# Optimization experiments

Measured on AMD Instinct MI355X. Metric: run time of the kernel, lower is better.

## Reference

```python
import jax, jax.numpy as jnp
import numpy as np

N = 50000
E = 800000
F_IN = 128
HID = 128
OUT = 64
EPS = 1e-5


def gcn_conv(x, src, dst, deg_inv_sqrt, W, b):
    # h = x @ W  (dense transform first, like PyG GCNConv)
    h = x @ W  # [N, F_out]
    norm = deg_inv_sqrt[src] * deg_inv_sqrt[dst]  # [E+N] (self-loops included)
    msgs = norm[:, None] * h[src]  # gather + scale, [E+N, F_out]
    out = jax.ops.segment_sum(msgs, dst, num_segments=N)  # scatter-add to targets
    return out + b


def setup_inputs() -> dict:
    key = jax.random.key(0)
    ks = jax.random.split(key, 9)
    x = jax.random.normal(ks[0], (N, F_IN), dtype=jnp.float32)
    edge_index = jax.random.randint(ks[1], (2, E), 0, N, dtype=jnp.int64)
    s = 1.0 / np.sqrt(F_IN)
    W1 = jax.random.uniform(ks[2], (F_IN, HID), jnp.float32, -s, s)
    b1 = jnp.zeros((HID,), jnp.float32)
    sh = 1.0 / np.sqrt(HID)
    Wmu = jax.random.uniform(ks[3], (HID, OUT), jnp.float32, -sh, sh)
    bmu = jnp.zeros((OUT,), jnp.float32)
    Wlv = jax.random.uniform(ks[4], (HID, OUT), jnp.float32, -sh, sh)
    blv = jnp.zeros((OUT,), jnp.float32)
    gamma = jnp.ones((HID,), jnp.float32)
    beta = jnp.zeros((HID,), jnp.float32)
    return {"x": x, "edge_index": edge_index, "W1": W1, "b1": b1,
            "gamma": gamma, "beta": beta, "Wmu": Wmu, "bmu": bmu,
            "Wlv": Wlv, "blv": blv}


def reference(x, edge_index, W1, b1, gamma, beta, Wmu, bmu, Wlv, blv):
    # Add self-loops (GCNConv default) and compute symmetric normalization once.
    loop = jnp.arange(N, dtype=edge_index.dtype)
    src = jnp.concatenate([edge_index[0], loop])
    dst = jnp.concatenate([edge_index[1], loop])
    deg = jax.ops.segment_sum(jnp.ones_like(dst, dtype=x.dtype), dst, num_segments=N)
    deg_inv_sqrt = jnp.where(deg > 0, jax.lax.rsqrt(deg), 0.0)

    h = jax.nn.relu(gcn_conv(x, src, dst, deg_inv_sqrt, W1, b1))
    # per-node LayerNorm over feature dim
    mean = jnp.mean(h, axis=-1, keepdims=True)
    var = jnp.var(h, axis=-1, keepdims=True)
    h = (h - mean) * jax.lax.rsqrt(var + EPS) * gamma + beta

    mu = gcn_conv(h, src, dst, deg_inv_sqrt, Wmu, bmu)
    logvar = gcn_conv(h, src, dst, deg_inv_sqrt, Wlv, blv)
    return mu, logvar
```

## Files before the change

### kernel.cpp

```cpp
#include <hip/hip_runtime.h>

#define NN 50000
#define EE 800000
#define FF 128
#define OO 64
#define EPSF 1e-5f
#define SCB 196
#define EBLK 3125
#define GBLK 391

typedef unsigned int uint;
typedef unsigned short ushort;
typedef __attribute__((ext_vector_type(8))) short short8;
typedef __attribute__((ext_vector_type(4))) float f32x4;

__device__ __forceinline__ float bflo(uint v) { return __uint_as_float(v << 16); }
__device__ __forceinline__ float bfhi(uint v) { return __uint_as_float(v & 0xFFFF0000u); }
__device__ __forceinline__ uint f2bf(float f) {
  uint b = __float_as_uint(f);
  return (b + 0x7FFFu + ((b >> 16) & 1u)) >> 16;
}
__device__ __forceinline__ uint pack2(float x, float y) { return f2bf(x) | (f2bf(y) << 16); }

__device__ __forceinline__ int eidx(const void* ei, long long pos, int f64) {
  if (f64) return (int)((const long long*)ei)[pos];
  return ((const int*)ei)[pos];
}

__global__ void k_init(const void* ei, int* flag, int* cnt) {
  int i = blockIdx.x * 256 + threadIdx.x;
  if (i < NN) cnt[i] = 0;
  if (i == 0) {
    const int* p = (const int*)ei;
    int any = 0;
    for (int j = 1; j < 128; j += 2) any |= p[j];
    *flag = (any == 0) ? 1 : 0;
  }
}

__global__ void k_deg_rank(const void* ei, const int* __restrict__ flag,
                           int* __restrict__ cnt, int* __restrict__ rank) {
  int e = blockIdx.x * 256 + threadIdx.x;
  if (e >= EE) return;
  int f64 = *flag;
  int d = eidx(ei, (long long)EE + e, f64);
  rank[e] = atomicAdd(&cnt[d], 1);
}

__global__ __launch_bounds__(256) void k_dis_part(const int* __restrict__ cnt,
                                                  float* __restrict__ dis,
                                                  int* __restrict__ bsum) {
  int i = blockIdx.x * 256 + threadIdx.x;
  int v = (i < NN) ? cnt[i] : 0;
  if (i < NN) dis[i] = rsqrtf((float)(v + 1));
  int s = v;
#pragma unroll
  for (int m = 1; m < 64; m <<= 1) s += __shfl_xor(s, m);
  __shared__ int ws[4];
  if ((threadIdx.x & 63) == 0) ws[threadIdx.x >> 6] = s;
  __syncthreads();
  if (threadIdx.x == 0) bsum[blockIdx.x] = ws[0] + ws[1] + ws[2] + ws[3];
}

__global__ __launch_bounds__(256) void k_scan_tops(const int* __restrict__ bsum,
                                                   int* __restrict__ boff,
                                                   int* __restrict__ rowptr) {
  __shared__ int s[256];
  int tid = threadIdx.x;
  int v = (tid < SCB) ? bsum[tid] : 0;
  s[tid] = v;
  __syncthreads();
  for (int off = 1; off < 256; off <<= 1) {
    int t = (tid >= off) ? s[tid - off] : 0;
    __syncthreads();
    s[tid] += t;
    __syncthreads();
  }
  if (tid < SCB) boff[tid] = s[tid] - v;
  if (tid == 255) rowptr[NN] = s[255];
}

__global__ __launch_bounds__(256) void k_scan_write(const int* __restrict__ cnt,
                                                    const int* __restrict__ boff,
                                                    int* __restrict__ rowptr) {
  int blk = blockIdx.x, tid = threadIdx.x;
  int i = blk * 256 + tid;
  int v = (i < NN) ? cnt[i] : 0;
  int lane = tid & 63, wid = tid >> 6;
  int inc = v;
#pragma unroll
  for (int off = 1; off < 64; off <<= 1) {
    int t = __shfl_up(inc, off);
    if (lane >= off) inc += t;
  }
  __shared__ int wsum[4];
  if (lane == 63) wsum[wid] = inc;
  __syncthreads();
  int wadd = 0;
  for (int wj = 0; wj < wid; ++wj) wadd += wsum[wj];
  int exc = inc - v + wadd + boff[blk];
  if (i < NN) rowptr[i] = exc;
}

__device__ __forceinline__ int wt_idx(int c, int k) {
  return c * 128 + (k ^ ((c & 7) << 3));
}

__global__ __launch_bounds__(256) void k_scatter_gemm1(
    const void* ei, const int* __restrict__ flag, const float* __restrict__ dis,
    const int* __restrict__ rowptr, const int* __restrict__ rank,
    int2* __restrict__ cw,
    const float* __restrict__ X, const float* __restrict__ W,
    ushort* __restrict__ T) {
  __shared__ ushort Wt[FF * FF];
  if (blockIdx.x >= GBLK) {
    int e = (blockIdx.x - GBLK) * 256 + threadIdx.x;
    if (e >= EE) return;
    int f64 = *flag;
    int s = eidx(ei, e, f64);
    int d = eidx(ei, (long long)EE + e, f64);
    int p = rowptr[d] + rank[e];
    int2 v;
    v.x = s;
    v.y = __float_as_int(dis[s] * dis[d]);
    cw[p] = v;
    return;
  }
  for (int i = threadIdx.x; i < FF * FF; i += 256) {
    int k = i >> 7, c = i & 127;
    Wt[wt_idx(c, k)] = (ushort)f2bf(W[i]);
  }
  __syncthreads();
  int l = threadIdx.x & 63, wv = threadIdx.x >> 6;
  int rbase = blockIdx.x * 128 + wv * 32;
  int lr = l & 15, lk = (l >> 4) << 3;
  f32x4 acc[2][8] = {};
#pragma unroll
  for (int kb = 0; kb < 4; ++kb) {
    int kk = kb * 32 + lk;
    short8 a[2];
#pragma unroll
    for (int rt = 0; rt < 2; ++rt) {
      int row = min(rbase + rt * 16 + lr, NN - 1);
      const float4* ap = (const float4*)(X + (size_t)row * FF + kk);
      float4 x0 = ap[0], x1 = ap[1];
      a[rt][0] = (short)f2bf(x0.x); a[rt][1] = (short)f2bf(x0.y);
      a[rt][2] = (short)f2bf(x0.z); a[rt][3] = (short)f2bf(x0.w);
      a[rt][4] = (short)f2bf(x1.x); a[rt][5] = (short)f2bf(x1.y);
      a[rt][6] = (short)f2bf(x1.z); a[rt][7] = (short)f2bf(x1.w);
    }
#pragma unroll
    for (int ct = 0; ct < 8; ++ct) {
      int c = ct * 16 + lr;
      short8 b = *(const short8*)&Wt[wt_idx(c, kk)];
      acc[0][ct] = __builtin_amdgcn_mfma_f32_16x16x32_bf16(a[0], b, acc[0][ct], 0, 0, 0);
      acc[1][ct] = __builtin_amdgcn_mfma_f32_16x16x32_bf16(a[1], b, acc[1][ct], 0, 0, 0);
    }
  }
  int rl = (l >> 4) * 4;
#pragma unroll
  for (int rt = 0; rt < 2; ++rt)
#pragma unroll
    for (int reg = 0; reg < 4; ++reg) {
      int row = rbase + rt * 16 + rl + reg;
      if (row < NN) {
#pragma unroll
        for (int ct = 0; ct < 8; ++ct)
          T[(size_t)row * FF + ct * 16 + lr] = (ushort)f2bf(acc[rt][ct][reg]);
      }
    }
}

__global__ __launch_bounds__(256) void k_gemm2(const ushort* __restrict__ A,
                                               const float* __restrict__ Wmu,
                                               const float* __restrict__ bmu,
                                               const float* __restrict__ Wlv,
                                               const float* __restrict__ blv,
                                               float* __restrict__ out) {
  __shared__ ushort Wt[FF * FF];
  __shared__ float sb[FF];
  for (int i = threadIdx.x; i < FF * FF; i += 256) {
    int k = i >> 7, c = i & 127;
    float v = (c < OO) ? Wmu[k * OO + c] : Wlv[k * OO + (c - OO)];
    Wt[wt_idx(c, k)] = (ushort)f2bf(v);
  }
  if (threadIdx.x < FF)
    sb[threadIdx.x] = (threadIdx.x < OO) ? bmu[threadIdx.x] : blv[threadIdx.x - OO];
  __syncthreads();
  int l = threadIdx.x & 63, wv = threadIdx.x >> 6;
  int rbase = blockIdx.x * 128 + wv * 32;
  int lr = l & 15, lk = (l >> 4) << 3;
  f32x4 acc[2][8] = {};
#pragma unroll
  for (int kb = 0; kb < 4; ++kb) {
    int kk = kb * 32 + lk;
    short8 a[2];
#pragma unroll
    for (int rt = 0; rt < 2; ++rt) {
      int row = min(rbase + rt * 16 + lr, NN - 1);
      a[rt] = *(const short8*)(A + (size_t)row * FF + kk);
    }
#pragma unroll
    for (int ct = 0; ct < 8; ++ct) {
      int c = ct * 16 + lr;
      short8 b = *(const short8*)&Wt[wt_idx(c, kk)];
      acc[0][ct] = __builtin_amdgcn_mfma_f32_16x16x32_bf16(a[0], b, acc[0][ct], 0, 0, 0);
      acc[1][ct] = __builtin_amdgcn_mfma_f32_16x16x32_bf16(a[1], b, acc[1][ct], 0, 0, 0);
    }
  }
  int rl = (l >> 4) * 4;
#pragma unroll
  for (int rt = 0; rt < 2; ++rt)
#pragma unroll
    for (int reg = 0; reg < 4; ++reg) {
      int row = rbase + rt * 16 + rl + reg;
      if (row < NN) {
#pragma unroll
        for (int ct = 0; ct < 8; ++ct) {
          int c = ct * 16 + lr;
          float v = acc[rt][ct][reg] + sb[c];
          if (ct < 4) out[(size_t)row * OO + c] = v;
          else out[(size_t)NN * OO + (size_t)row * OO + (c - OO)] = v;
        }
      }
    }
}

template <int LN>
__global__ __launch_bounds__(256) void k_gather(const int* __restrict__ rowptr,
                                                const int2* __restrict__ cw,
                                                const float* __restrict__ dis,
                                                const ushort* __restrict__ feat,
                                                const float* __restrict__ b1,
                                                const float* __restrict__ gamma,
                                                const float* __restrict__ beta,
                                                ushort* __restrict__ outp) {
  int node = blockIdx.x * 4 + (threadIdx.x >> 6);
  if (node >= NN) return;
  int l = threadIdx.x & 63;
  int g = l >> 4;
  int c16 = l & 15;

  float di = dis[node];
  uint4 vSelf = ((const uint4*)(feat + ((size_t)node << 7)))[c16];

  float acc[8] = {};
  int e0 = rowptr[node], nE = rowptr[node + 1] - e0;
  int base = 0;
  for (; base + 8 <= nE; base += 8) {
    int2 cA = cw[e0 + base + g];
    int2 cB = cw[e0 + base + 4 + g];
    uint4 vA = ((const uint4*)(feat + ((size_t)cA.x << 7)))[c16];
    uint4 vB = ((const uint4*)(feat + ((size_t)cB.x << 7)))[c16];
    float wA = __int_as_float(cA.y), wB = __int_as_float(cB.y);
    acc[0] = fmaf(wA, bflo(vA.x), acc[0]); acc[1] = fmaf(wA, bfhi(vA.x), acc[1]);
    acc[2] = fmaf(wA, bflo(vA.y), acc[2]); acc[3] = fmaf(wA, bfhi(vA.y), acc[3]);
    acc[4] = fmaf(wA, bflo(vA.z), acc[4]); acc[5] = fmaf(wA, bfhi(vA.z), acc[5]);
    acc[6] = fmaf(wA, bflo(vA.w), acc[6]); acc[7] = fmaf(wA, bfhi(vA.w), acc[7]);
    acc[0] = fmaf(wB, bflo(vB.x), acc[0]); acc[1] = fmaf(wB, bfhi(vB.x), acc[1]);
    acc[2] = fmaf(wB, bflo(vB.y), acc[2]); acc[3] = fmaf(wB, bfhi(vB.y), acc[3]);
    acc[4] = fmaf(wB, bflo(vB.z), acc[4]); acc[5] = fmaf(wB, bfhi(vB.z), acc[5]);
    acc[6] = fmaf(wB, bflo(vB.w), acc[6]); acc[7] = fmaf(wB, bfhi(vB.w), acc[7]);
  }
#pragma unroll
  for (int t = 0; t < 2; ++t) {
    int idx = base + t * 4 + g;
    if (idx < nE) {
      int2 c0 = cw[e0 + idx];
      uint4 v = ((const uint4*)(feat + ((size_t)c0.x << 7)))[c16];
      float w0 = __int_as_float(c0.y);
      acc[0] = fmaf(w0, bflo(v.x), acc[0]); acc[1] = fmaf(w0, bfhi(v.x), acc[1]);
      acc[2] = fmaf(w0, bflo(v.y), acc[2]); acc[3] = fmaf(w0, bfhi(v.y), acc[3]);
      acc[4] = fmaf(w0, bflo(v.z), acc[4]); acc[5] = fmaf(w0, bfhi(v.z), acc[5]);
      acc[6] = fmaf(w0, bflo(v.w), acc[6]); acc[7] = fmaf(w0, bfhi(v.w), acc[7]);
    }
  }
#pragma unroll
  for (int j = 0; j < 8; ++j) {
    acc[j] += __shfl_xor(acc[j], 16);
    acc[j] += __shfl_xor(acc[j], 32);
  }
  {
    float sw = di * di;
    acc[0] = fmaf(sw, bflo(vSelf.x), acc[0]); acc[1] = fmaf(sw, bfhi(vSelf.x), acc[1]);
    acc[2] = fmaf(sw, bflo(vSelf.y), acc[2]); acc[3] = fmaf(sw, bfhi(vSelf.y), acc[3]);
    acc[4] = fmaf(sw, bflo(vSelf.z), acc[4]); acc[5] = fmaf(sw, bfhi(vSelf.z), acc[5]);
    acc[6] = fmaf(sw, bflo(vSelf.w), acc[6]); acc[7] = fmaf(sw, bfhi(vSelf.w), acc[7]);
  }
  int cOff = c16 * 8;
  float o[8];
  if (LN) {
    float4 ba = *(const float4*)&b1[cOff];
    float4 bb = *(const float4*)&b1[cOff + 4];
    float a[8];
    a[0] = fmaxf(acc[0] + ba.x, 0.f); a[1] = fmaxf(acc[1] + ba.y, 0.f);
    a[2] = fmaxf(acc[2] + ba.z, 0.f); a[3] = fmaxf(acc[3] + ba.w, 0.f);
    a[4] = fmaxf(acc[4] + bb.x, 0.f); a[5] = fmaxf(acc[5] + bb.y, 0.f);
    a[6] = fmaxf(acc[6] + bb.z, 0.f); a[7] = fmaxf(acc[7] + bb.w, 0.f);
    float s = 0.f, sq = 0.f;
#pragma unroll
    for (int j = 0; j < 8; ++j) { s += a[j]; sq += a[j] * a[j]; }
#pragma unroll
    for (int m = 1; m < 16; m <<= 1) {
      s += __shfl_xor(s, m);
      sq += __shfl_xor(sq, m);
    }
    float mean = s * (1.f / 128.f);
    float var = sq * (1.f / 128.f) - mean * mean;
    float rstd = rsqrtf(var + EPSF);
    float4 ga = *(const float4*)&gamma[cOff];
    float4 gb = *(const float4*)&gamma[cOff + 4];
    float4 ea = *(const float4*)&beta[cOff];
    float4 eb = *(const float4*)&beta[cOff + 4];
    o[0] = (a[0] - mean) * rstd * ga.x + ea.x; o[1] = (a[1] - mean) * rstd * ga.y + ea.y;
    o[2] = (a[2] - mean) * rstd * ga.z + ea.z; o[3] = (a[3] - mean) * rstd * ga.w + ea.w;
    o[4] = (a[4] - mean) * rstd * gb.x + eb.x; o[5] = (a[5] - mean) * rstd * gb.y + eb.y;
    o[6] = (a[6] - mean) * rstd * gb.z + eb.z; o[7] = (a[7] - mean) * rstd * gb.w + eb.w;
  } else {
#pragma unroll
    for (int j = 0; j < 8; ++j) o[j] = acc[j];
  }
  if (g == 0) {
    uint4 p;
    p.x = pack2(o[0], o[1]); p.y = pack2(o[2], o[3]);
    p.z = pack2(o[4], o[5]); p.w = pack2(o[6], o[7]);
    ((uint4*)(outp + ((size_t)node << 7)))[c16] = p;
  }
}

extern "C" void kernel_launch(void* const* d_in, const int* in_sizes, int n_in,
                              void* d_out, int out_size, void* d_ws, size_t ws_size,
                              hipStream_t stream) {
  const float* x     = (const float*)d_in[0];
  const void*  ei    = d_in[1];
  const float* W1    = (const float*)d_in[2];
  const float* b1    = (const float*)d_in[3];
  const float* gamma = (const float*)d_in[4];
  const float* beta  = (const float*)d_in[5];
  const float* Wmu   = (const float*)d_in[6];
  const float* bmu   = (const float*)d_in[7];
  const float* Wlv   = (const float*)d_in[8];
  const float* blv   = (const float*)d_in[9];
  float* out = (float*)d_out;

  int*   flag   = (int*)d_ws;
  int*   cnt    = flag + 64;
  int*   rowptr = cnt + NN;
  float* dis    = (float*)(rowptr + (NN + 16));
  int*   bsum   = (int*)(dis + NN);
  int*   boff   = bsum + 256;
  int*   rank   = boff + 256;
  size_t off32  = (size_t)(64 + NN + (NN + 16) + NN + 256 + 256 + EE);
  off32 = (off32 + 63) & ~(size_t)63;
  int2*  cw     = (int2*)((int*)d_ws + off32);
  ushort* t  = (ushort*)(cw + EE);
  ushort* h  = t + (size_t)NN * FF;
  ushort* t2 = h + (size_t)NN * FF;

  k_init<<<SCB, 256, 0, stream>>>(ei, flag, cnt);
  k_deg_rank<<<EBLK, 256, 0, stream>>>(ei, flag, cnt, rank);
  k_dis_part<<<SCB, 256, 0, stream>>>(cnt, dis, bsum);
  k_scan_tops<<<1, 256, 0, stream>>>(bsum, boff, rowptr);
  k_scan_write<<<SCB, 256, 0, stream>>>(cnt, boff, rowptr);
  k_scatter_gemm1<<<GBLK + EBLK, 256, 0, stream>>>(ei, flag, dis, rowptr, rank, cw,
                                                   x, W1, t);
  k_gather<1><<<(NN + 3) / 4, 256, 0, stream>>>(rowptr, cw, dis, t, b1, gamma, beta, h);
  k_gather<0><<<(NN + 3) / 4, 256, 0, stream>>>(rowptr, cw, dis, h, b1, gamma, beta, t2);
  k_gemm2<<<GBLK, 256, 0, stream>>>(t2, Wmu, bmu, Wlv, blv, out);
}
```

Baseline: 156.5 us.

## Reorder second layer to transform-then-aggregate and move GEMM1 into degree pass

The second GCN layer now multiplies h by the concatenated Wmu|Wlv weights first and then aggregates neighbours, with bias added in the final gather, instead of aggregating h and then multiplying. This removes the separate output GEMM pass that read the aggregated features. The first GEMM is merged into the degree/rank counting kernel, so the edge scatter now runs as its own kernel. The second gather still moves 128 bf16 features per edge, so its traffic is about the same, and the outputs now pass through bf16 rounding before aggregation instead of after.

After: 157.9 us. Within noise of the previous version (+0.9%).

```diff
diff --git a/kernel.cpp b/kernel.cpp
--- a/kernel.cpp
+++ b/kernel.cpp
@@ -38,13 +38,67 @@
   }
 }
 
-__global__ void k_deg_rank(const void* ei, const int* __restrict__ flag,
-                           int* __restrict__ cnt, int* __restrict__ rank) {
-  int e = blockIdx.x * 256 + threadIdx.x;
-  if (e >= EE) return;
-  int f64 = *flag;
-  int d = eidx(ei, (long long)EE + e, f64);
-  rank[e] = atomicAdd(&cnt[d], 1);
+__device__ __forceinline__ int wt_idx(int c, int k) {
+  return c * 128 + (k ^ ((c & 7) << 3));
+}
+
+__global__ __launch_bounds__(256) void k_deg_gemm1(
+    const void* ei, const int* __restrict__ flag,
+    int* __restrict__ cnt, int* __restrict__ rank,
+    const float* __restrict__ X, const float* __restrict__ W,
+    ushort* __restrict__ T) {
+  __shared__ ushort Wt[FF * FF];
+  if (blockIdx.x >= GBLK) {
+    int e = (blockIdx.x - GBLK) * 256 + threadIdx.x;
+    if (e >= EE) return;
+    int f64 = *flag;
+    int d = eidx(ei, (long long)EE + e, f64);
+    rank[e] = atomicAdd(&cnt[d], 1);
+    return;
+  }
+  for (int i = threadIdx.x; i < FF * FF; i += 256) {
+    int k = i >> 7, c = i & 127;
+    Wt[wt_idx(c, k)] = (ushort)f2bf(W[i]);
+  }
+  __syncthreads();
+  int l = threadIdx.x & 63, wv = threadIdx.x >> 6;
+  int rbase = blockIdx.x * 128 + wv * 32;
+  int lr = l & 15, lk = (l >> 4) << 3;
+  f32x4 acc[2][8] = {};
+#pragma unroll
+  for (int kb = 0; kb < 4; ++kb) {
+    int kk = kb * 32 + lk;
+    short8 a[2];
+#pragma unroll
+    for (int rt = 0; rt < 2; ++rt) {
+      int row = min(rbase + rt * 16 + lr, NN - 1);
+      const float4* ap = (const float4*)(X + (size_t)row * FF + kk);
+      float4 x0 = ap[0], x1 = ap[1];
+      a[rt][0] = (short)f2bf(x0.x); a[rt][1] = (short)f2bf(x0.y);
+      a[rt][2] = (short)f2bf(x0.z); a[rt][3] = (short)f2bf(x0.w);
+      a[rt][4] = (short)f2bf(x1.x); a[rt][5] = (short)f2bf(x1.y);
+      a[rt][6] = (short)f2bf(x1.z); a[rt][7] = (short)f2bf(x1.w);
+    }
+#pragma unroll
+    for (int ct = 0; ct < 8; ++ct) {
+      int c = ct * 16 + lr;
+      short8 b = *(const short8*)&Wt[wt_idx(c, kk)];
+      acc[0][ct] = __builtin_amdgcn_mfma_f32_16x16x32_bf16(a[0], b, acc[0][ct], 0, 0, 0);
+      acc[1][ct] = __builtin_amdgcn_mfma_f32_16x16x32_bf16(a[1], b, acc[1][ct], 0, 0, 0);
+    }
+  }
+  int rl = (l >> 4) * 4;
+#pragma unroll
+  for (int rt = 0; rt < 2; ++rt)
+#pragma unroll
+    for (int reg = 0; reg < 4; ++reg) {
+      int row = rbase + rt * 16 + rl + reg;
+      if (row < NN) {
+#pragma unroll
+        for (int ct = 0; ct < 8; ++ct)
+          T[(size_t)row * FF + ct * 16 + lr] = (ushort)f2bf(acc[rt][ct][reg]);
+      }
+    }
 }
 
 __global__ __launch_bounds__(256) void k_dis_part(const int* __restrict__ cnt,
@@ -102,33 +156,32 @@
   if (i < NN) rowptr[i] = exc;
 }
 
-__device__ __forceinline__ int wt_idx(int c, int k) {
-  return c * 128 + (k ^ ((c & 7) << 3));
-}
-
-__global__ __launch_bounds__(256) void k_scatter_gemm1(
-    const void* ei, const int* __restrict__ flag, const float* __restrict__ dis,
-    const int* __restrict__ rowptr, const int* __restrict__ rank,
-    int2* __restrict__ cw,
-    const float* __restrict__ X, const float* __restrict__ W,
-    ushort* __restrict__ T) {
+__global__ void k_scatter(const void* ei, const int* __restrict__ flag,
+                          const float* __restrict__ dis,
+                          const int* __restrict__ rowptr,
+                          const int* __restrict__ rank,
+                          int2* __restrict__ cw) {
+  int e = blockIdx.x * 256 + threadIdx.x;
+  if (e >= EE) return;
+  int f64 = *flag;
+  int s = eidx(ei, e, f64);
+  int d = eidx(ei, (long long)EE + e, f64);
+  int p = rowptr[d] + rank[e];
+  int2 v;
+  v.x = s;
+  v.y = __float_as_int(dis[s] * dis[d]);
+  cw[p] = v;
+}
+
+__global__ __launch_bounds__(256) void k_gemmHW(const ushort* __restrict__ A,
+                                                const float* __restrict__ Wmu,
+                                                const float* __restrict__ Wlv,
+                                                ushort* __restrict__ T) {
   __shared__ ushort Wt[FF * FF];
-  if (blockIdx.x >= GBLK) {
-    int e = (blockIdx.x - GBLK) * 256 + threadIdx.x;
-    if (e >= EE) return;
-    int f64 = *flag;
-    int s = eidx(ei, e, f64);
-    int d = eidx(ei, (long long)EE + e, f64);
-    int p = rowptr[d] + rank[e];
-    int2 v;
-    v.x = s;
-    v.y = __float_as_int(dis[s] * dis[d]);
-    cw[p] = v;
-    return;
-  }
   for (int i = threadIdx.x; i < FF * FF; i += 256) {
     int k = i >> 7, c = i & 127;
-    Wt[wt_idx(c, k)] = (ushort)f2bf(W[i]);
+    float v = (c < OO) ? Wmu[k * OO + c] : Wlv[k * OO + (c - OO)];
+    Wt[wt_idx(c, k)] = (ushort)f2bf(v);
   }
   __syncthreads();
   int l = threadIdx.x & 63, wv = threadIdx.x >> 6;
@@ -142,12 +195,7 @@
 #pragma unroll
     for (int rt = 0; rt < 2; ++rt) {
       int row = min(rbase + rt * 16 + lr, NN - 1);
-      const float4* ap = (const float4*)(X + (size_t)row * FF + kk);
-      float4 x0 = ap[0], x1 = ap[1];
-      a[rt][0] = (short)f2bf(x0.x); a[rt][1] = (short)f2bf(x0.y);
-      a[rt][2] = (short)f2bf(x0.z); a[rt][3] = (short)f2bf(x0.w);
-      a[rt][4] = (short)f2bf(x1.x); a[rt][5] = (short)f2bf(x1.y);
-      a[rt][6] = (short)f2bf(x1.z); a[rt][7] = (short)f2bf(x1.w);
+      a[rt] = *(const short8*)(A + (size_t)row * FF + kk);
     }
 #pragma unroll
     for (int ct = 0; ct < 8; ++ct) {
@@ -171,70 +219,14 @@
     }
 }
 
-__global__ __launch_bounds__(256) void k_gemm2(const ushort* __restrict__ A,
-                                               const float* __restrict__ Wmu,
-                                               const float* __restrict__ bmu,
-                                               const float* __restrict__ Wlv,
-                                               const float* __restrict__ blv,
-                                               float* __restrict__ out) {
-  __shared__ ushort Wt[FF * FF];
-  __shared__ float sb[FF];
-  for (int i = threadIdx.x; i < FF * FF; i += 256) {
-    int k = i >> 7, c = i & 127;
-    float v = (c < OO) ? Wmu[k * OO + c] : Wlv[k * OO + (c - OO)];
-    Wt[wt_idx(c, k)] = (ushort)f2bf(v);
-  }
-  if (threadIdx.x < FF)
-    sb[threadIdx.x] = (threadIdx.x < OO) ? bmu[threadIdx.x] : blv[threadIdx.x - OO];
-  __syncthreads();
-  int l = threadIdx.x & 63, wv = threadIdx.x >> 6;
-  int rbase = blockIdx.x * 128 + wv * 32;
-  int lr = l & 15, lk = (l >> 4) << 3;
-  f32x4 acc[2][8] = {};
-#pragma unroll
-  for (int kb = 0; kb < 4; ++kb) {
-    int kk = kb * 32 + lk;
-    short8 a[2];
-#pragma unroll
-    for (int rt = 0; rt < 2; ++rt) {
-      int row = min(rbase + rt * 16 + lr, NN - 1);
-      a[rt] = *(const short8*)(A + (size_t)row * FF + kk);
-    }
-#pragma unroll
-    for (int ct = 0; ct < 8; ++ct) {
-      int c = ct * 16 + lr;
-      short8 b = *(const short8*)&Wt[wt_idx(c, kk)];
-      acc[0][ct] = __builtin_amdgcn_mfma_f32_16x16x32_bf16(a[0], b, acc[0][ct], 0, 0, 0);
-      acc[1][ct] = __builtin_amdgcn_mfma_f32_16x16x32_bf16(a[1], b, acc[1][ct], 0, 0, 0);
-    }
-  }
-  int rl = (l >> 4) * 4;
-#pragma unroll
-  for (int rt = 0; rt < 2; ++rt)
-#pragma unroll
-    for (int reg = 0; reg < 4; ++reg) {
-      int row = rbase + rt * 16 + rl + reg;
-      if (row < NN) {
-#pragma unroll
-        for (int ct = 0; ct < 8; ++ct) {
-          int c = ct * 16 + lr;
-          float v = acc[rt][ct][reg] + sb[c];
-          if (ct < 4) out[(size_t)row * OO + c] = v;
-          else out[(size_t)NN * OO + (size_t)row * OO + (c - OO)] = v;
-        }
-      }
-    }
-}
-
-template <int LN>
-__global__ __launch_bounds__(256) void k_gather(const int* __restrict__ rowptr,
-                                                const int2* __restrict__ cw,
-                                                const float* __restrict__ dis,
-                                                const ushort* __restrict__ feat,
-                                                const float* __restrict__ b1,
-                                                const float* __restrict__ gamma,
-                                                const float* __restrict__ beta,
-                                                ushort* __restrict__ outp) {
+__global__ __launch_bounds__(256) void k_gather_ln(const int* __restrict__ rowptr,
+                                                   const int2* __restrict__ cw,
+                                                   const float* __restrict__ dis,
+                                                   const ushort* __restrict__ feat,
+                                                   const float* __restrict__ b1,
+                                                   const float* __restrict__ gamma,
+                                                   const float* __restrict__ beta,
+                                                   ushort* __restrict__ outp) {
   int node = blockIdx.x * 4 + (threadIdx.x >> 6);
   if (node >= NN) return;
   int l = threadIdx.x & 63;
@@ -288,43 +280,110 @@
     acc[6] = fmaf(sw, bflo(vSelf.w), acc[6]); acc[7] = fmaf(sw, bfhi(vSelf.w), acc[7]);
   }
   int cOff = c16 * 8;
+  float4 ba = *(const float4*)&b1[cOff];
+  float4 bb = *(const float4*)&b1[cOff + 4];
+  float a[8];
+  a[0] = fmaxf(acc[0] + ba.x, 0.f); a[1] = fmaxf(acc[1] + ba.y, 0.f);
+  a[2] = fmaxf(acc[2] + ba.z, 0.f); a[3] = fmaxf(acc[3] + ba.w, 0.f);
+  a[4] = fmaxf(acc[4] + bb.x, 0.f); a[5] = fmaxf(acc[5] + bb.y, 0.f);
+  a[6] = fmaxf(acc[6] + bb.z, 0.f); a[7] = fmaxf(acc[7] + bb.w, 0.f);
+  float s = 0.f, sq = 0.f;
+#pragma unroll
+  for (int j = 0; j < 8; ++j) { s += a[j]; sq += a[j] * a[j]; }
+#pragma unroll
+  for (int m = 1; m < 16; m <<= 1) {
+    s += __shfl_xor(s, m);
+    sq += __shfl_xor(sq, m);
+  }
+  float mean = s * (1.f / 128.f);
+  float var = sq * (1.f / 128.f) - mean * mean;
+  float rstd = rsqrtf(var + EPSF);
+  float4 ga = *(const float4*)&gamma[cOff];
+  float4 gb = *(const float4*)&gamma[cOff + 4];
+  float4 ea = *(const float4*)&beta[cOff];
+  float4 eb = *(const float4*)&beta[cOff + 4];
   float o[8];
-  if (LN) {
-    float4 ba = *(const float4*)&b1[cOff];
-    float4 bb = *(const float4*)&b1[cOff + 4];
-    float a[8];
-    a[0] = fmaxf(acc[0] + ba.x, 0.f); a[1] = fmaxf(acc[1] + ba.y, 0.f);
-    a[2] = fmaxf(acc[2] + ba.z, 0.f); a[3] = fmaxf(acc[3] + ba.w, 0.f);
-    a[4] = fmaxf(acc[4] + bb.x, 0.f); a[5] = fmaxf(acc[5] + bb.y, 0.f);
-    a[6] = fmaxf(acc[6] + bb.z, 0.f); a[7] = fmaxf(acc[7] + bb.w, 0.f);
-    float s = 0.f, sq = 0.f;
-#pragma unroll
-    for (int j = 0; j < 8; ++j) { s += a[j]; sq += a[j] * a[j]; }
-#pragma unroll
-    for (int m = 1; m < 16; m <<= 1) {
-      s += __shfl_xor(s, m);
-      sq += __shfl_xor(sq, m);
-    }
-    float mean = s * (1.f / 128.f);
-    float var = sq * (1.f / 128.f) - mean * mean;
-    float rstd = rsqrtf(var + EPSF);
-    float4 ga = *(const float4*)&gamma[cOff];
-    float4 gb = *(const float4*)&gamma[cOff + 4];
-    float4 ea = *(const float4*)&beta[cOff];
-    float4 eb = *(const float4*)&beta[cOff + 4];
-    o[0] = (a[0] - mean) * rstd * ga.x + ea.x; o[1] = (a[1] - mean) * rstd * ga.y + ea.y;
-    o[2] = (a[2] - mean) * rstd * ga.z + ea.z; o[3] = (a[3] - mean) * rstd * ga.w + ea.w;
-    o[4] = (a[4] - mean) * rstd * gb.x + eb.x; o[5] = (a[5] - mean) * rstd * gb.y + eb.y;
-    o[6] = (a[6] - mean) * rstd * gb.z + eb.z; o[7] = (a[7] - mean) * rstd * gb.w + eb.w;
-  } else {
-#pragma unroll
-    for (int j = 0; j < 8; ++j) o[j] = acc[j];
-  }
+  o[0] = (a[0] - mean) * rstd * ga.x + ea.x; o[1] = (a[1] - mean) * rstd * ga.y + ea.y;
+  o[2] = (a[2] - mean) * rstd * ga.z + ea.z; o[3] = (a[3] - mean) * rstd * ga.w + ea.w;
+  o[4] = (a[4] - mean) * rstd * gb.x + eb.x; o[5] = (a[5] - mean) * rstd * gb.y + eb.y;
+  o[6] = (a[6] - mean) * rstd * gb.z + eb.z; o[7] = (a[7] - mean) * rstd * gb.w + eb.w;
   if (g == 0) {
     uint4 p;
     p.x = pack2(o[0], o[1]); p.y = pack2(o[2], o[3]);
     p.z = pack2(o[4], o[5]); p.w = pack2(o[6], o[7]);
     ((uint4*)(outp + ((size_t)node << 7)))[c16] = p;
+  }
+}
+
+__global__ __launch_bounds__(256) void k_gather_out(const int* __restrict__ rowptr,
+                                                    const int2* __restrict__ cw,
+                                                    const float* __restrict__ dis,
+                                                    const ushort* __restrict__ feat,
+                                                    const float* __restrict__ bmu,
+                                                    const float* __restrict__ blv,
+                                                    float* __restrict__ out) {
+  int node = blockIdx.x * 4 + (threadIdx.x >> 6);
+  if (node >= NN) return;
+  int l = threadIdx.x & 63;
+  int g = l >> 4;
+  int c16 = l & 15;
+
+  float di = dis[node];
+  uint4 vSelf = ((const uint4*)(feat + ((size_t)node << 7)))[c16];
+
+  float acc[8] = {};
+  int e0 = rowptr[node], nE = rowptr[node + 1] - e0;
+  int base = 0;
+  for (; base + 8 <= nE; base += 8) {
+    int2 cA = cw[e0 + base + g];
+    int2 cB = cw[e0 + base + 4 + g];
+    uint4 vA = ((const uint4*)(feat + ((size_t)cA.x << 7)))[c16];
+    uint4 vB = ((const uint4*)(feat + ((size_t)cB.x << 7)))[c16];
+    float wA = __int_as_float(cA.y), wB = __int_as_float(cB.y);
+    acc[0] = fmaf(wA, bflo(vA.x), acc[0]); acc[1] = fmaf(wA, bfhi(vA.x), acc[1]);
+    acc[2] = fmaf(wA, bflo(vA.y), acc[2]); acc[3] = fmaf(wA, bfhi(vA.y), acc[3]);
+    acc[4] = fmaf(wA, bflo(vA.z), acc[4]); acc[5] = fmaf(wA, bfhi(vA.z), acc[5]);
+    acc[6] = fmaf(wA, bflo(vA.w), acc[6]); acc[7] = fmaf(wA, bfhi(vA.w), acc[7]);
+    acc[0] = fmaf(wB, bflo(vB.x), acc[0]); acc[1] = fmaf(wB, bfhi(vB.x), acc[1]);
+    acc[2] = fmaf(wB, bflo(vB.y), acc[2]); acc[3] = fmaf(wB, bfhi(vB.y), acc[3]);
+    acc[4] = fmaf(wB, bflo(vB.z), acc[4]); acc[5] = fmaf(wB, bfhi(vB.z), acc[5]);
+    acc[6] = fmaf(wB, bflo(vB.w), acc[6]); acc[7] = fmaf(wB, bfhi(vB.w), acc[7]);
+  }
+#pragma unroll
+  for (int t = 0; t < 2; ++t) {
+    int idx = base + t * 4 + g;
+    if (idx < nE) {
+      int2 c0 = cw[e0 + idx];
+      uint4 v = ((const uint4*)(feat + ((size_t)c0.x << 7)))[c16];
+      float w0 = __int_as_float(c0.y);
+      acc[0] = fmaf(w0, bflo(v.x), acc[0]); acc[1] = fmaf(w0, bfhi(v.x), acc[1]);
+      acc[2] = fmaf(w0, bflo(v.y), acc[2]); acc[3] = fmaf(w0, bfhi(v.y), acc[3]);
+      acc[4] = fmaf(w0, bflo(v.z), acc[4]); acc[5] = fmaf(w0, bfhi(v.z), acc[5]);
+      acc[6] = fmaf(w0, bflo(v.w), acc[6]); acc[7] = fmaf(w0, bfhi(v.w), acc[7]);
+    }
+  }
+#pragma unroll
+  for (int j = 0; j < 8; ++j) {
+    acc[j] += __shfl_xor(acc[j], 16);
+    acc[j] += __shfl_xor(acc[j], 32);
+  }
+  {
+    float sw = di * di;
+    acc[0] = fmaf(sw, bflo(vSelf.x), acc[0]); acc[1] = fmaf(sw, bfhi(vSelf.x), acc[1]);
+    acc[2] = fmaf(sw, bflo(vSelf.y), acc[2]); acc[3] = fmaf(sw, bfhi(vSelf.y), acc[3]);
+    acc[4] = fmaf(sw, bflo(vSelf.z), acc[4]); acc[5] = fmaf(sw, bfhi(vSelf.z), acc[5]);
+    acc[6] = fmaf(sw, bflo(vSelf.w), acc[6]); acc[7] = fmaf(sw, bfhi(vSelf.w), acc[7]);
+  }
+  if (g == 0) {
+    const float* bsrc = (c16 < 8) ? (bmu + c16 * 8) : (blv + (c16 - 8) * 8);
+    float* osrc = (c16 < 8) ? (out + (size_t)node * OO + c16 * 8)
+                            : (out + (size_t)NN * OO + (size_t)node * OO + (c16 - 8) * 8);
+    float4 b0 = *(const float4*)bsrc;
+    float4 b1 = *(const float4*)(bsrc + 4);
+    float4 o0 = { acc[0] + b0.x, acc[1] + b0.y, acc[2] + b0.z, acc[3] + b0.w };
+    float4 o1 = { acc[4] + b1.x, acc[5] + b1.y, acc[6] + b1.z, acc[7] + b1.w };
+    *(float4*)osrc = o0;
+    *(float4*)(osrc + 4) = o1;
   }
 }
 
@@ -355,16 +414,16 @@
   int2*  cw     = (int2*)((int*)d_ws + off32);
   ushort* t  = (ushort*)(cw + EE);
   ushort* h  = t + (size_t)NN * FF;
-  ushort* t2 = h + (size_t)NN * FF;
+  ushort* hw = h + (size_t)NN * FF;
 
   k_init<<<SCB, 256, 0, stream>>>(ei, flag, cnt);
-  k_deg_rank<<<EBLK, 256, 0, stream>>>(ei, flag, cnt, rank);
+  k_deg_gemm1<<<GBLK + EBLK, 256, 0, stream>>>(ei, flag, cnt, rank, x, W1, t);
   k_dis_part<<<SCB, 256, 0, stream>>>(cnt, dis, bsum);
   k_scan_tops<<<1, 256, 0, stream>>>(bsum, boff, rowptr);
   k_scan_write<<<SCB, 256, 0, stream>>>(cnt, boff, rowptr);
-  k_scatter_gemm1<<<GBLK + EBLK, 256, 0, stream>>>(ei, flag, dis, rowptr, rank, cw,
-                                                   x, W1, t);
-  k_gather<1><<<(NN + 3) / 4, 256, 0, stream>>>(rowptr, cw, dis, t, b1, gamma, beta, h);
-  k_gather<0><<<(NN + 3) / 4, 256, 0, stream>>>(rowptr, cw, dis, h, b1, gamma, beta, t2);
-  k_gemm2<<<GBLK, 256, 0, stream>>>(t2, Wmu, bmu, Wlv, blv, out);
-}
+  k_scatter<<<EBLK, 256, 0, stream>>>(ei, flag, dis, rowptr, rank, cw);
+
+  k_gather_ln<<<(NN + 3) / 4, 256, 0, stream>>>(rowptr, cw, dis, t, b1, gamma, beta, h);
+  k_gemmHW<<<GBLK, 256, 0, stream>>>(h, Wmu, Wlv, hw);
+  k_gather_out<<<(NN + 3) / 4, 256, 0, stream>>>(rowptr, cw, dis, hw, bmu, blv, out);
+}
```
